# Optimization experiments

Hardware: AMD Instinct MI355X
Metric: run time of the kernel (lower is better)

The kernel has to match this reference:

```python
import jax, jax.numpy as jnp
import numpy as np

L, H, NH, HD, F, B, S = 32, 1024, 16, 64, 2048, 2, 2048
HPH = H // NH  # hidden per attention head (hyena column split)
EPS = 1e-6
BLOCK = {0:'HCS',4:'HCS',7:'HCS',11:'HCS',14:'HCS',18:'HCS',21:'HCS',25:'HCS',28:'HCS',
         1:'HCM',5:'HCM',8:'HCM',12:'HCM',15:'HCM',19:'HCM',22:'HCM',26:'HCM',29:'HCM',
         2:'HCL',6:'HCL',9:'HCL',13:'HCL',16:'HCL',20:'HCL',23:'HCL',27:'HCL',30:'HCL',
         3:'ATT',10:'ATT',17:'ATT',24:'ATT',31:'ATT'}

def rmsnorm(x, w):
    return x * jax.lax.rsqrt(jnp.mean(x * x, -1, keepdims=True) + EPS) * w

def step_fir(u, state, w, b, flip=False, gated=False):
    # u:[B,C]  state:[B,C,cache]  w:[C,Lf]  b:[C]  (single-token FIR step)
    cache = state.shape[-1]
    w = w[:, ::-1][:, -(cache + 1):] if flip else w[:, :cache + 1]
    y = w[:, -1] * u + jnp.sum(state * w[:, :-1], -1)
    y = y + (b * u if gated else b)
    return y

def split3(z):
    # column_split_hyena=True path of _interleave_split
    r = z.reshape(z.shape[0], NH, 3 * HPH)
    x2 = r[:, :, :HPH].reshape(z.shape[0], H)
    x1 = r[:, :, HPH:2 * HPH].reshape(z.shape[0], H)
    v = r[:, :, 2 * HPH:].reshape(z.shape[0], H)
    return x2, x1, v

def mlp(x, W1, W2):
    return jax.nn.gelu(x @ W1.T) @ W2.T

def fir_block(x, n1, n2, pW, pb, oW, ob, W1, W2, sfw, sfb, h, D, fstate, istate, flip, gated):
    xn = rmsnorm(x, n1)
    z = xn @ pW.T + pb                 # [B,1,3H]
    u = z[:, -1]                       # [B,3H]
    zp = step_fir(u, fstate, sfw, sfb)
    x2, x1, v = split3(zp)
    y = step_fir(x1 * v, istate, h, D, flip=flip, gated=gated)
    y = (y * x2)[:, None]              # [B,1,H]
    x = y @ oW.T + ob + x
    return mlp(rmsnorm(x, n2), W1, W2) + x

def hcl_block(x, n1, n2, pW, pb, oW, ob, W1, W2, sfw, sfb, log_poles, residues, D, fstate, iir):
    xn = rmsnorm(x, n1)
    z = xn @ pW.T + pb
    u = z[:, -1]
    zp = step_fir(u, fstate, sfw, sfb)
    x2, x1, v = split3(zp)
    x1v = x1 * v
    iir_new = jnp.exp(log_poles) * iir + x1v[..., None]   # [B,H,SS] single-step IIR update
    res = jnp.sum(residues * iir_new, -1)
    y = (x2 * (res + D * x1v))[:, None]
    x = y @ oW.T + ob + x
    return mlp(rmsnorm(x, n2), W1, W2) + x

def att_block(x, n1, n2, qW, qb, oW, ob, W1, W2, kc, vc, cos, sin, pos):
    xn = rmsnorm(x, n1)
    qkv = (xn @ qW.T + qb).reshape(B, 1, 3, NH, HD)
    q, k, v = qkv[:, :, 0], qkv[:, :, 1], qkv[:, :, 2]
    c = jnp.concatenate([cos[pos], cos[pos]])  # [HD]
    s = jnp.concatenate([sin[pos], sin[pos]])
    rot = lambda t: jnp.concatenate([-t[..., HD // 2:], t[..., :HD // 2]], -1)
    q = q * c + rot(q) * s
    k = k * c + rot(k) * s
    kc = kc.at[:, pos].set(k[:, 0])  # KV-cache scatter write at current position
    vc = vc.at[:, pos].set(v[:, 0])
    scores = jnp.einsum('bohd,bshd->bhos', q, kc) * (HD ** -0.5)
    scores = jnp.where(jnp.arange(S) > pos, -10000.0, scores)
    aw = jax.nn.softmax(scores, -1)
    ctx = jnp.einsum('bhos,bshd->bohd', aw, vc).reshape(B, 1, H)
    x = ctx @ oW.T + ob + x
    return mlp(rmsnorm(x, n2), W1, W2) + x

def forward(x, position, norm1_w, norm2_w, proj_W, proj_b, out_W, out_b, mlp_W1, mlp_W2,
            sf_w, sf_b, hcs_h, hcs_D, hcm_h, hcm_D, hcl_logpoles, hcl_residues, hcl_D,
            fir_state, hcs_state, hcm_state, iir_state, k_cache, v_cache, rope_cos, rope_sin):
    att = 0
    for i in range(L):  # loop over 32 structurally distinct layers (static)
        t = BLOCK[i]
        cm = (norm1_w[i], norm2_w[i], proj_W[i], proj_b[i], out_W[i], out_b[i], mlp_W1[i], mlp_W2[i])
        if t == 'HCS':
            x = fir_block(x, *cm, sf_w[i], sf_b[i], hcs_h[i], hcs_D[i], fir_state[i], hcs_state[i], False, False)
        elif t == 'HCM':
            x = fir_block(x, *cm, sf_w[i], sf_b[i], hcm_h[i], hcm_D[i], fir_state[i], hcm_state[i], True, True)
        elif t == 'HCL':
            x = hcl_block(x, *cm, sf_w[i], sf_b[i], hcl_logpoles[i], hcl_residues[i], hcl_D[i], fir_state[i], iir_state[i])
        else:
            x = att_block(x, *cm, k_cache[att], v_cache[att], rope_cos, rope_sin, position)
            att += 1
    return x

def setup_inputs():
    key = jax.random.key(0)
    ks = jax.random.split(key, 24)
    g = lambda k, shape, sc: jax.random.normal(k, shape, jnp.float32) * sc
    inv_freq = 1.0 / (10000.0 ** (np.arange(0, HD, 2, dtype=np.float32) / HD))
    ang = np.arange(S, dtype=np.float32)[:, None] * inv_freq[None, :]
    return {
        'x': g(ks[0], (B, 1, H), 1.0),
        'position': 1024,
        'norm1_w': jnp.ones((L, H), jnp.float32),
        'norm2_w': jnp.ones((L, H), jnp.float32),
        'proj_W': g(ks[1], (L, 3 * H, H), H ** -0.5),
        'proj_b': jnp.zeros((L, 3 * H), jnp.float32),
        'out_W': g(ks[2], (L, H, H), 0.2 * H ** -0.5),
        'out_b': jnp.zeros((L, H), jnp.float32),
        'mlp_W1': g(ks[3], (L, F, H), H ** -0.5),
        'mlp_W2': g(ks[4], (L, H, F), 0.2 * F ** -0.5),
        'sf_w': g(ks[5], (L, 3 * H, 3), 0.4),
        'sf_b': g(ks[6], (L, 3 * H), 0.02),
        'hcs_h': g(ks[7], (L, H, 7), 0.2),
        'hcs_D': g(ks[8], (L, H), 0.2),
        'hcm_h': g(ks[9], (L, H, 128), 0.04),
        'hcm_D': g(ks[10], (L, H), 0.2),
        'hcl_logpoles': -jax.random.uniform(ks[11], (L, H, 16), jnp.float32, 0.01, 2.0),
        'hcl_residues': g(ks[12], (L, H, 16), 0.1),
        'hcl_D': g(ks[13], (L, H), 0.2),
        'fir_state': g(ks[14], (L, B, 3 * H, 2), 0.5),
        'hcs_state': g(ks[15], (L, B, H, 6), 0.5),
        'hcm_state': g(ks[16], (L, B, H, 127), 0.5),
        'iir_state': g(ks[17], (L, B, H, 16), 0.5),
        'k_cache': g(ks[18], (5, B, S, NH, HD), 1.0),
        'v_cache': g(ks[19], (5, B, S, NH, HD), 1.0),
        'rope_cos': jnp.asarray(np.cos(ang)),
        'rope_sin': jnp.asarray(np.sin(ang)),
    }

def reference(x, position, norm1_w, norm2_w, proj_W, proj_b, out_W, out_b, mlp_W1, mlp_W2,
              sf_w, sf_b, hcs_h, hcs_D, hcm_h, hcm_D, hcl_logpoles, hcl_residues, hcl_D,
              fir_state, hcs_state, hcm_state, iir_state, k_cache, v_cache, rope_cos, rope_sin):
    return forward(x, position, norm1_w, norm2_w, proj_W, proj_b, out_W, out_b, mlp_W1, mlp_W2,
                   sf_w, sf_b, hcs_h, hcs_D, hcm_h, hcm_D, hcl_logpoles, hcl_residues, hcl_D,
                   fir_state, hcs_state, hcm_state, iir_state, k_cache, v_cache, rope_cos, rope_sin)
```

## Files before the change

### kernel.cpp

```cpp
#include <hip/hip_runtime.h>
#include <hip/hip_bf16.h>
#include <math.h>

#define LAYERS 32
#define H      1024
#define H3     3072
#define NHEADS 16
#define HDIM   64
#define FF     2048
#define BATCH  2
#define SEQ    2048
#define EPSF   1e-6f

__device__ __forceinline__ float wredSum(float v) {
#pragma unroll
  for (int m = 32; m >= 1; m >>= 1) v += __shfl_xor(v, m, 64);
  return v;
}
__device__ __forceinline__ float wredMax(float v) {
#pragma unroll
  for (int m = 32; m >= 1; m >>= 1) v = fmaxf(v, __shfl_xor(v, m, 64));
  return v;
}
__device__ __forceinline__ float gelu_t(float x) {
  return 0.5f * x * (1.0f + tanhf(0.7978845608028654f * (x + 0.044715f * x * x * x)));
}

__global__ __launch_bounds__(256) void prep_kernel(
    const float* __restrict__ sf_w, const float* __restrict__ sf_b,
    const float* __restrict__ fir_state,
    const float* __restrict__ hcs_h, const float* __restrict__ hcs_D, const float* __restrict__ hcs_state,
    const float* __restrict__ hcm_h, const float* __restrict__ hcm_D, const float* __restrict__ hcm_state,
    const float* __restrict__ lp, const float* __restrict__ resd, const float* __restrict__ hcl_D,
    const float* __restrict__ iir,
    unsigned long long kbits,
    float* __restrict__ sfd, float* __restrict__ sfc,
    float* __restrict__ mix0, float* __restrict__ mix1)
{
  int blk = blockIdx.x, tid = threadIdx.x;
  if (blk < 768) {
    int idx = blk * 256 + tid;
    int i = idx / (BATCH * H3);
    int r = idx % (BATCH * H3);
    int b = r / H3, ch = r % H3;
    const float* fs = fir_state + ((size_t)(i * BATCH + b) * H3 + ch) * 2;
    const float* sw = sf_w + ((size_t)i * H3 + ch) * 3;
    sfd[idx] = fs[0] * sw[0] + fs[1] * sw[1] + sf_b[i * H3 + ch];
    if (b == 0) sfc[i * H3 + ch] = sw[2];
  } else if (blk < 1024) {
    int idx = (blk - 768) * 256 + tid;
    int i = idx >> 11;
    int r = idx & 2047;
    int b = r >> 10, c = r & 1023;
    int kind = (int)((kbits >> (2 * i)) & 3ull);
    if (kind == 0) {
      const float* st = hcs_state + ((size_t)(i * BATCH + b) * H + c) * 6;
      const float* hh = hcs_h + ((size_t)i * H + c) * 7;
      float acc = 0.f;
#pragma unroll
      for (int k = 0; k < 6; k++) acc += st[k] * hh[k];
      mix0[idx] = acc + hcs_D[i * H + c];
      if (b == 0) mix1[i * H + c] = hh[6];
    } else if (kind == 2) {
      const float* ii = iir + ((size_t)(i * BATCH + b) * H + c) * 16;
      const float* lpp = lp + ((size_t)i * H + c) * 16;
      const float* rs = resd + ((size_t)i * H + c) * 16;
      float acc = 0.f, rsum = 0.f;
#pragma unroll
      for (int k = 0; k < 16; k++) { float rv = rs[k]; acc += rv * expf(lpp[k]) * ii[k]; rsum += rv; }
      mix0[idx] = acc;
      if (b == 0) mix1[i * H + c] = rsum + hcl_D[i * H + c];
    }
  } else {
    int w = tid >> 6, lane = tid & 63;
    int widx = (blk - 1024) * 4 + w;
    if (widx < 9 * BATCH * H) {
      int li = widx >> 11;
      int r = widx & 2047;
      int b = r >> 10, c = r & 1023;
      int i = (li >> 1) * 7 + ((li & 1) ? 5 : 1);
      const float* st = hcm_state + ((size_t)(i * BATCH + b) * H + c) * 127;
      const float* hh = hcm_h + ((size_t)i * H + c) * 128;
      float acc = 0.f;
      int k = lane;
      if (k < 127) acc += st[k] * hh[127 - k];
      k = lane + 64;
      if (k < 127) acc += st[k] * hh[127 - k];
      acc = wredSum(acc);
      if (lane == 0) {
        mix0[(i * BATCH + b) * H + c] = acc;
        if (b == 0) mix1[i * H + c] = hh[0] + hcm_D[i * H + c];
      }
    }
  }
}

template<int ROWS, bool GELU, bool HASBIAS>
__global__ __launch_bounds__(256) void gemv_norm_kernel(
    const float* __restrict__ x, const float* __restrict__ nw,
    const float* __restrict__ W, const float* __restrict__ bias,
    float* __restrict__ out)
{
  __shared__ alignas(16) float xe[BATCH][H];
  __shared__ float red[8];
  __shared__ float scl[BATCH];
  int tid = threadIdx.x, lane = tid & 63, w = tid >> 6;
  int r0 = blockIdx.x * 8 + w * 2;
  const float4* row0 = (const float4*)(W + (size_t)r0 * H);
  const float4* row1 = (const float4*)(W + (size_t)(r0 + 1) * H);
  float4 wa[4], wb[4];
#pragma unroll
  for (int j = 0; j < 4; j++) { wa[j] = row0[lane + 64 * j]; wb[j] = row1[lane + 64 * j]; }

  float ss0 = 0.f, ss1 = 0.f;
#pragma unroll
  for (int it = 0; it < 8; it++) {
    int e = tid + it * 256;
    int b = e >> 10, c = e & 1023;
    float xv = x[b * H + c];
    xe[b][c] = xv * nw[c];
    if (it < 4) ss0 += xv * xv; else ss1 += xv * xv;
  }
  ss0 = wredSum(ss0); ss1 = wredSum(ss1);
  if (lane == 0) { red[w] = ss0; red[4 + w] = ss1; }
  __syncthreads();
  if (tid == 0) {
    scl[0] = rsqrtf((red[0] + red[1] + red[2] + red[3]) * (1.0f / H) + EPSF);
    scl[1] = rsqrtf((red[4] + red[5] + red[6] + red[7]) * (1.0f / H) + EPSF);
  }
  __syncthreads();

  float a00 = 0.f, a01 = 0.f, a10 = 0.f, a11 = 0.f;
  const float4* x0 = (const float4*)xe[0];
  const float4* x1 = (const float4*)xe[1];
#pragma unroll
  for (int j = 0; j < 4; j++) {
    float4 h0 = x0[lane + 64 * j], h1 = x1[lane + 64 * j];
    a00 += wa[j].x * h0.x + wa[j].y * h0.y + wa[j].z * h0.z + wa[j].w * h0.w;
    a01 += wa[j].x * h1.x + wa[j].y * h1.y + wa[j].z * h1.z + wa[j].w * h1.w;
    a10 += wb[j].x * h0.x + wb[j].y * h0.y + wb[j].z * h0.z + wb[j].w * h0.w;
    a11 += wb[j].x * h1.x + wb[j].y * h1.y + wb[j].z * h1.z + wb[j].w * h1.w;
  }
  a00 = wredSum(a00); a01 = wredSum(a01); a10 = wredSum(a10); a11 = wredSum(a11);
  if (lane == 0) {
    float s0 = scl[0], s1 = scl[1];
    float b0 = HASBIAS ? bias[r0] : 0.f;
    float b1 = HASBIAS ? bias[r0 + 1] : 0.f;
    float v00 = a00 * s0 + b0, v01 = a01 * s1 + b0;
    float v10 = a10 * s0 + b1, v11 = a11 * s1 + b1;
    if (GELU) { v00 = gelu_t(v00); v01 = gelu_t(v01); v10 = gelu_t(v10); v11 = gelu_t(v11); }
    out[0 * ROWS + r0] = v00;
    out[1 * ROWS + r0] = v01;
    out[0 * ROWS + r0 + 1] = v10;
    out[1 * ROWS + r0 + 1] = v11;
  }
}

__global__ __launch_bounds__(256) void mix_out_kernel(
    int kind,
    const float* __restrict__ z, const float* __restrict__ sfdL, const float* __restrict__ sfcL,
    const float* __restrict__ mix0L, const float* __restrict__ mix1L,
    const float* __restrict__ attP,
    const float* __restrict__ oW, const float* __restrict__ ob,
    const float* __restrict__ x_in, float* __restrict__ x_out)
{
  __shared__ alignas(16) float y[BATCH][H];
  int tid = threadIdx.x, lane = tid & 63, w = tid >> 6;
  int r0 = blockIdx.x * 8 + w * 2;
  const float4* row0 = (const float4*)(oW + (size_t)r0 * H);
  const float4* row1 = (const float4*)(oW + (size_t)(r0 + 1) * H);
  float4 wa[4], wb[4];
#pragma unroll
  for (int j = 0; j < 4; j++) { wa[j] = row0[lane + 64 * j]; wb[j] = row1[lane + 64 * j]; }

  if (kind < 3) {
#pragma unroll
    for (int it = 0; it < 8; it++) {
      int e = tid + it * 256;
      int b = e >> 10, c = e & 1023;
      int n = c >> 6, d = c & 63;
      int base = n * 192 + d;
      float x2 = sfcL[base] * z[b * H3 + base] + sfdL[b * H3 + base];
      float x1 = sfcL[base + 64] * z[b * H3 + base + 64] + sfdL[b * H3 + base + 64];
      float vv = sfcL[base + 128] * z[b * H3 + base + 128] + sfdL[b * H3 + base + 128];
      float t = x1 * vv;
      y[b][c] = (mix1L[c] * t + mix0L[b * H + c]) * x2;
    }
  } else {
#pragma unroll
    for (int it = 0; it < 8; it++) {
      int e = tid + it * 256;
      int b = e >> 10, c = e & 1023;
      int n = c >> 6, d = c & 63;
      float M = -1e30f;
#pragma unroll
      for (int sp = 0; sp < 8; sp++) M = fmaxf(M, attP[((sp * BATCH + b) * NHEADS + n) * 66 + 64]);
      float Ls = 0.f, num = 0.f;
#pragma unroll
      for (int sp = 0; sp < 8; sp++) {
        const float* P = attP + ((sp * BATCH + b) * NHEADS + n) * 66;
        float wgt = expf(P[64] - M);
        Ls += wgt * P[65];
        num += wgt * P[d];
      }
      y[b][c] = num / Ls;
    }
  }
  __syncthreads();

  float a00 = 0.f, a01 = 0.f, a10 = 0.f, a11 = 0.f;
  const float4* y0 = (const float4*)y[0];
  const float4* y1 = (const float4*)y[1];
#pragma unroll
  for (int j = 0; j < 4; j++) {
    float4 h0 = y0[lane + 64 * j], h1 = y1[lane + 64 * j];
    a00 += wa[j].x * h0.x + wa[j].y * h0.y + wa[j].z * h0.z + wa[j].w * h0.w;
    a01 += wa[j].x * h1.x + wa[j].y * h1.y + wa[j].z * h1.z + wa[j].w * h1.w;
    a10 += wb[j].x * h0.x + wb[j].y * h0.y + wb[j].z * h0.z + wb[j].w * h0.w;
    a11 += wb[j].x * h1.x + wb[j].y * h1.y + wb[j].z * h1.z + wb[j].w * h1.w;
  }
  a00 = wredSum(a00); a01 = wredSum(a01); a10 = wredSum(a10); a11 = wredSum(a11);
  if (lane == 0) {
    x_out[0 * H + r0]     = a00 + ob[r0]     + x_in[0 * H + r0];
    x_out[1 * H + r0]     = a01 + ob[r0]     + x_in[1 * H + r0];
    x_out[0 * H + r0 + 1] = a10 + ob[r0 + 1] + x_in[0 * H + r0 + 1];
    x_out[1 * H + r0 + 1] = a11 + ob[r0 + 1] + x_in[1 * H + r0 + 1];
  }
}

__global__ __launch_bounds__(256) void gemv_mlp2_kernel(
    const float* __restrict__ h, const float* __restrict__ W2,
    const float* __restrict__ x_in, float* __restrict__ x_out)
{
  __shared__ alignas(16) float hs[BATCH][FF];
  int tid = threadIdx.x, lane = tid & 63, w = tid >> 6;
  int r = blockIdx.x * 4 + w;
  const float4* row = (const float4*)(W2 + (size_t)r * FF);
  float4 wv[8];
#pragma unroll
  for (int j = 0; j < 8; j++) wv[j] = row[lane + 64 * j];
#pragma unroll
  for (int it = 0; it < 16; it++) {
    int e = tid + it * 256;
    int b = e >> 11, c = e & 2047;
    hs[b][c] = h[b * FF + c];
  }
  __syncthreads();
  float a0 = 0.f, a1 = 0.f;
  const float4* h0 = (const float4*)hs[0];
  const float4* h1 = (const float4*)hs[1];
#pragma unroll
  for (int j = 0; j < 8; j++) {
    float4 p = h0[lane + 64 * j], q = h1[lane + 64 * j];
    a0 += wv[j].x * p.x + wv[j].y * p.y + wv[j].z * p.z + wv[j].w * p.w;
    a1 += wv[j].x * q.x + wv[j].y * q.y + wv[j].z * q.z + wv[j].w * q.w;
  }
  a0 = wredSum(a0); a1 = wredSum(a1);
  if (lane == 0) {
    x_out[0 * H + r] = a0 + x_in[0 * H + r];
    x_out[1 * H + r] = a1 + x_in[1 * H + r];
  }
}

__global__ __launch_bounds__(256) void attn_kernel(
    const float* __restrict__ z, const int* __restrict__ posp,
    const float* __restrict__ kc, const float* __restrict__ vc,
    const float* __restrict__ cosT, const float* __restrict__ sinT,
    float* __restrict__ P)
{
  int sp = blockIdx.x & 7, n = (blockIdx.x >> 3) & 15, b = blockIdx.x >> 7;
  int pos = *posp;
  __shared__ alignas(16) float q_s[HDIM], k_s[HDIM], v_s[HDIM];
  __shared__ float eg[256];
  __shared__ float redA[4];
  __shared__ alignas(16) float osum[4][HDIM];
  int tid = threadIdx.x, lane = tid & 63, w = tid >> 6;

  if (tid < 64) {
    int d = tid, j = d & 31;
    float cs = cosT[pos * 32 + j], sn = sinT[pos * 32 + j];
    float qv = z[b * H3 + n * 64 + d];
    float qo = z[b * H3 + n * 64 + ((d + 32) & 63)];
    q_s[d] = ((d < 32) ? (qv * cs - qo * sn) : (qv * cs + qo * sn)) * 0.125f;
    float kv = z[b * H3 + 1024 + n * 64 + d];
    float ko = z[b * H3 + 1024 + n * 64 + ((d + 32) & 63)];
    k_s[d] = (d < 32) ? (kv * cs - ko * sn) : (kv * cs + ko * sn);
    v_s[d] = z[b * H3 + 2048 + n * 64 + d];
  }
  __syncthreads();

  int s = sp * 256 + tid;
  float logit = -1e30f;
  if (s <= pos) {
    const float4* k4 = (s == pos) ? (const float4*)k_s
                                  : (const float4*)(kc + (((size_t)b * SEQ + s) * NHEADS + n) * HDIM);
    const float4* q4 = (const float4*)q_s;
    float acc = 0.f;
#pragma unroll
    for (int j = 0; j < 16; j++) {
      float4 kk = k4[j], qq = q4[j];
      acc += kk.x * qq.x + kk.y * qq.y + kk.z * qq.z + kk.w * qq.w;
    }
    logit = acc;
  }
  float m = wredMax(logit);
  if (lane == 0) redA[w] = m;
  __syncthreads();
  m = fmaxf(fmaxf(redA[0], redA[1]), fmaxf(redA[2], redA[3]));
  float e = (s <= pos) ? expf(logit - m) : 0.f;
  eg[tid] = e;
  float ps = wredSum(e);
  __syncthreads();
  if (lane == 0) redA[w] = ps;
  __syncthreads();
  float lsum = redA[0] + redA[1] + redA[2] + redA[3];

  int dgrp = lane & 15, srow = lane >> 4;
  float4 acc = make_float4(0.f, 0.f, 0.f, 0.f);
#pragma unroll 4
  for (int it = 0; it < 16; it++) {
    int sl = w * 64 + it * 4;
    if (sp * 256 + sl > pos) break;
    int sli = sl + srow;
    int ss = sp * 256 + sli;
    float ev = eg[sli];
    const float4* v4 = (ss == pos) ? (const float4*)v_s
                                   : (const float4*)(vc + (((size_t)b * SEQ + ss) * NHEADS + n) * HDIM);
    float4 vv = v4[dgrp];
    acc.x += ev * vv.x; acc.y += ev * vv.y; acc.z += ev * vv.z; acc.w += ev * vv.w;
  }
#pragma unroll
  for (int mm = 16; mm <= 32; mm <<= 1) {
    acc.x += __shfl_xor(acc.x, mm, 64);
    acc.y += __shfl_xor(acc.y, mm, 64);
    acc.z += __shfl_xor(acc.z, mm, 64);
    acc.w += __shfl_xor(acc.w, mm, 64);
  }
  if (srow == 0) ((float4*)osum[w])[dgrp] = acc;
  __syncthreads();
  float* Pp = P + ((size_t)(sp * BATCH + b) * NHEADS + n) * 66;
  if (tid < 64) Pp[tid] = osum[0][tid] + osum[1][tid] + osum[2][tid] + osum[3][tid];
  if (tid == 64) Pp[64] = m;
  if (tid == 65) Pp[65] = lsum;
}

extern "C" void kernel_launch(void* const* d_in, const int* in_sizes, int n_in,
                              void* d_out, int out_size, void* d_ws, size_t ws_size,
                              hipStream_t stream) {
  (void)in_sizes; (void)n_in; (void)out_size; (void)ws_size;
  const float* x0    = (const float*)d_in[0];
  const int*   posp  = (const int*)d_in[1];
  const float* n1    = (const float*)d_in[2];
  const float* n2    = (const float*)d_in[3];
  const float* pW    = (const float*)d_in[4];
  const float* pb    = (const float*)d_in[5];
  const float* oW    = (const float*)d_in[6];
  const float* ob    = (const float*)d_in[7];
  const float* W1    = (const float*)d_in[8];
  const float* W2    = (const float*)d_in[9];
  const float* sfw   = (const float*)d_in[10];
  const float* sfb   = (const float*)d_in[11];
  const float* hcs_h = (const float*)d_in[12];
  const float* hcs_D = (const float*)d_in[13];
  const float* hcm_h = (const float*)d_in[14];
  const float* hcm_D = (const float*)d_in[15];
  const float* lp    = (const float*)d_in[16];
  const float* resd  = (const float*)d_in[17];
  const float* hclD  = (const float*)d_in[18];
  const float* fir   = (const float*)d_in[19];
  const float* hcsS  = (const float*)d_in[20];
  const float* hcmS  = (const float*)d_in[21];
  const float* iir   = (const float*)d_in[22];
  const float* kc    = (const float*)d_in[23];
  const float* vc    = (const float*)d_in[24];
  const float* cosT  = (const float*)d_in[25];
  const float* sinT  = (const float*)d_in[26];

  float* ws    = (float*)d_ws;
  float* xbuf0 = ws;
  float* xbuf1 = ws + 2048;
  float* zbuf  = ws + 4096;
  float* hbuf  = ws + 10240;
  float* attP  = ws + 14336;
  float* sfd   = ws + 31232;
  float* sfc   = ws + 227840;
  float* mix0  = ws + 326144;
  float* mix1  = ws + 391680;

  static const int KIND[LAYERS] = {0,1,2,3,0,1,2,0,1,2,3,0,1,2,0,1,2,3,0,1,2,0,1,2,3,0,1,2,0,1,2,3};
  unsigned long long kbits = 0ull;
  for (int i = 0; i < LAYERS; i++) kbits |= ((unsigned long long)KIND[i]) << (2 * i);

  prep_kernel<<<5632, 256, 0, stream>>>(sfw, sfb, fir, hcs_h, hcs_D, hcsS,
      hcm_h, hcm_D, hcmS, lp, resd, hclD, iir, kbits, sfd, sfc, mix0, mix1);

  const float* xsrc = x0;
  int att = 0;
  for (int i = 0; i < LAYERS; i++) {
    gemv_norm_kernel<H3, false, true><<<H3 / 8, 256, 0, stream>>>(
        xsrc, n1 + i * H, pW + (size_t)i * H3 * H, pb + i * H3, zbuf);
    if (KIND[i] == 3) {
      attn_kernel<<<256, 256, 0, stream>>>(
          zbuf, posp, kc + (size_t)att * BATCH * SEQ * NHEADS * HDIM,
          vc + (size_t)att * BATCH * SEQ * NHEADS * HDIM, cosT, sinT, attP);
      att++;
    }
    mix_out_kernel<<<H / 8, 256, 0, stream>>>(
        KIND[i], zbuf, sfd + (size_t)i * BATCH * H3, sfc + (size_t)i * H3,
        mix0 + (size_t)i * BATCH * H, mix1 + (size_t)i * H, attP,
        oW + (size_t)i * H * H, ob + i * H, xsrc, xbuf1);
    gemv_norm_kernel<FF, true, false><<<FF / 8, 256, 0, stream>>>(
        xbuf1, n2 + i * H, W1 + (size_t)i * FF * H, nullptr, hbuf);
    gemv_mlp2_kernel<<<H / 4, 256, 0, stream>>>(
        hbuf, W2 + (size_t)i * H * FF, xbuf1, (i == 31) ? (float*)d_out : xbuf0);
    xsrc = xbuf0;
  }
}
```

Before: 702.8 us.

## Replace per-layer kernel launches with a persistent cooperative megakernel using grid barriers

Replaces the roughly 130 small per-layer kernel launches with one persistent cooperative kernel that walks all 32 layers. Stages are separated by a custom atomic grid barrier whose counters prep_kernel zeroes. The hyena FIR/mix elementwise step is fused into the projection GEMV epilogue, with projection rows reordered so each block gets matching x2/x1/v rows. Attention is re-split into 512 tasks. This removes launch overhead and inter-kernel gaps, but adds barrier spin costs and relies on all workgroups being co-resident.

```diff
diff --git a/kernel.cpp b/kernel.cpp
--- a/kernel.cpp
+++ b/kernel.cpp
@@ -11,6 +11,9 @@
 #define BATCH  2
 #define SEQ    2048
 #define EPSF   1e-6f
+#define NBAR   160
+
+__constant__ int d_KIND[LAYERS] = {0,1,2,3,0,1,2,0,1,2,3,0,1,2,0,1,2,3,0,1,2,0,1,2,3,0,1,2,0,1,2,3};
 
 __device__ __forceinline__ float wredSum(float v) {
 #pragma unroll
@@ -24,6 +27,369 @@
 }
 __device__ __forceinline__ float gelu_t(float x) {
   return 0.5f * x * (1.0f + tanhf(0.7978845608028654f * (x + 0.044715f * x * x * x)));
+}
+
+struct NS   { float xe[2][1024]; float red[16]; float scl[2]; float p[6][4][2]; };
+struct W2S  { float hs[2][2048]; float pr[2][8][2]; };
+struct OUTS { float ys[2][1024]; float pr[2][4][2]; };
+struct ATTS { float q[64]; float k[64]; float v[64]; float e[128]; float red[16]; float osum[8][64]; };
+union SH { NS ns; W2S w2; OUTS o; ATTS att; };
+
+struct MegaArgs {
+  const float* x0; const int* posp;
+  const float* n1; const float* n2;
+  const float* pW; const float* pb; const float* oW; const float* ob;
+  const float* W1; const float* W2;
+  const float* sfc; const float* sfd; const float* mix0; const float* mix1;
+  const float* kc; const float* vc; const float* cosT; const float* sinT;
+  float* z; float* y; float* xA; float* xB; float* xM; float* h; float* attP;
+  int* bar; float* out; int nwg;
+};
+
+__device__ __forceinline__ void gridbar(int* bar, int st, int wg, int nwg) {
+  __syncthreads();
+  if (threadIdx.x == 0) {
+    int* cnt  = bar + st * 8;
+    int* flag = bar + NBAR * 8 + st;
+    __hip_atomic_fetch_add(&cnt[wg & 7], 1, __ATOMIC_RELEASE, __HIP_MEMORY_SCOPE_AGENT);
+    if (wg == 0) {
+      int s;
+      do {
+        s = 0;
+#pragma unroll
+        for (int i = 0; i < 8; i++)
+          s += __hip_atomic_load(&cnt[i], __ATOMIC_RELAXED, __HIP_MEMORY_SCOPE_AGENT);
+      } while (s < nwg);
+      __hip_atomic_store(flag, 1, __ATOMIC_RELEASE, __HIP_MEMORY_SCOPE_AGENT);
+    } else {
+      while (__hip_atomic_load(flag, __ATOMIC_RELAXED, __HIP_MEMORY_SCOPE_AGENT) == 0) {}
+    }
+    __builtin_amdgcn_fence(__ATOMIC_ACQUIRE, "agent");
+  }
+  __syncthreads();
+}
+
+__device__ __forceinline__ void block_norm(const float* __restrict__ xin,
+                                           const float* __restrict__ nw, SH& sh) {
+  int tid = threadIdx.x, lane = tid & 63, wave = tid >> 6;
+  float4 xv = ((const float4*)xin)[tid];
+  int b = tid >> 8, ci = tid & 255;
+  float4 nv = ((const float4*)nw)[ci];
+  float ss = xv.x * xv.x + xv.y * xv.y + xv.z * xv.z + xv.w * xv.w;
+  ((float4*)&sh.ns.xe[b][ci << 2])[0] =
+      make_float4(xv.x * nv.x, xv.y * nv.y, xv.z * nv.z, xv.w * nv.w);
+  ss = wredSum(ss);
+  if (lane == 0) sh.ns.red[wave] = ss;
+  __syncthreads();
+  if (threadIdx.x == 0) {
+    sh.ns.scl[0] = rsqrtf((sh.ns.red[0] + sh.ns.red[1] + sh.ns.red[2] + sh.ns.red[3]) * (1.0f / 1024.f) + EPSF);
+    sh.ns.scl[1] = rsqrtf((sh.ns.red[4] + sh.ns.red[5] + sh.ns.red[6] + sh.ns.red[7]) * (1.0f / 1024.f) + EPSF);
+  }
+  __syncthreads();
+}
+
+__device__ __forceinline__ void stageP(const MegaArgs& a, SH& sh, int wg, int nwg,
+                                       int layer, int kind, const float* xin) {
+  block_norm(xin, a.n1 + layer * H, sh);
+  const float* W  = a.pW + (size_t)layer * H3 * H;
+  const float* pb = a.pb + layer * H3;
+  const float* sfcL = a.sfc + (size_t)layer * H3;
+  const float* sfdL = a.sfd + (size_t)layer * 2 * H3;
+  const float* mix0L = a.mix0 + (size_t)layer * 2 * H;
+  const float* mix1L = a.mix1 + (size_t)layer * H;
+  int tid = threadIdx.x, lane = tid & 63, wave = tid >> 6;
+  for (int rb = wg; rb < 512; rb += nwg) {
+    int n = rb >> 5, d0 = (rb & 31) << 1;
+    float part[3][2];
+    float4 wv[3];
+#pragma unroll
+    for (int k = 0; k < 3; k++) {
+      int t = wave + 8 * k, j = t >> 2, ch = t & 3;
+      int grow = (kind == 3) ? (rb * 6 + j) : (n * 192 + (j >> 1) * 64 + d0 + (j & 1));
+      wv[k] = *(const float4*)(W + (size_t)grow * H + (ch << 8) + (lane << 2));
+    }
+#pragma unroll
+    for (int k = 0; k < 3; k++) {
+      int ch = (wave + 8 * k) & 3;
+      float4 xa = *(const float4*)&sh.ns.xe[0][(ch << 8) + (lane << 2)];
+      float4 xb = *(const float4*)&sh.ns.xe[1][(ch << 8) + (lane << 2)];
+      part[k][0] = wv[k].x * xa.x + wv[k].y * xa.y + wv[k].z * xa.z + wv[k].w * xa.w;
+      part[k][1] = wv[k].x * xb.x + wv[k].y * xb.y + wv[k].z * xb.z + wv[k].w * xb.w;
+    }
+#pragma unroll
+    for (int k = 0; k < 3; k++) {
+      float s0 = wredSum(part[k][0]);
+      float s1 = wredSum(part[k][1]);
+      int t = wave + 8 * k, j = t >> 2, ch = t & 3;
+      if (lane == 0) { sh.ns.p[j][ch][0] = s0; sh.ns.p[j][ch][1] = s1; }
+    }
+    __syncthreads();
+    if (wave == 0) {
+      if (lane < 48) {
+        int j = lane >> 3, b = (lane >> 2) & 1, ch = lane & 3;
+        float v = sh.ns.p[j][ch][b];
+        v += __shfl_xor(v, 1, 64);
+        v += __shfl_xor(v, 2, 64);
+        if (ch == 0) {
+          int grow = (kind == 3) ? (rb * 6 + j) : (n * 192 + (j >> 1) * 64 + d0 + (j & 1));
+          float zraw = v * sh.ns.scl[b] + pb[grow];
+          if (kind == 3) {
+            a.z[b * H3 + grow] = zraw;
+          } else {
+            sh.ns.p[j][0][b] = sfcL[grow] * zraw + sfdL[b * H3 + grow];
+          }
+        }
+      }
+      if (kind != 3 && lane < 4) {
+        int q = lane & 1, b = lane >> 1;
+        float x2 = sh.ns.p[0 + q][0][b];
+        float x1 = sh.ns.p[2 + q][0][b];
+        float vv = sh.ns.p[4 + q][0][b];
+        int c = n * 64 + d0 + q;
+        float t = x1 * vv;
+        a.y[b * H + c] = (mix1L[c] * t + mix0L[b * H + c]) * x2;
+      }
+    }
+    __syncthreads();
+  }
+}
+
+__device__ __forceinline__ void stageA(const MegaArgs& a, SH& sh, int wg, int nwg, int att) {
+  int tid = threadIdx.x, lane = tid & 63;
+  int pos = a.posp[0];
+  int ck = (pos + 16) >> 4;
+  const float* kcL = a.kc + (size_t)att * BATCH * SEQ * NHEADS * HDIM;
+  const float* vcL = a.vc + (size_t)att * BATCH * SEQ * NHEADS * HDIM;
+  for (int task = wg; task < 512; task += nwg) {
+    int sp = task & 15, n = (task >> 4) & 15, b = task >> 8;
+    int s0 = sp * ck;
+    int send = min(s0 + ck, pos + 1);
+    if (tid < 64) {
+      int d = tid, jr = d & 31;
+      float cs = a.cosT[pos * 32 + jr], sn = a.sinT[pos * 32 + jr];
+      float qv = a.z[b * H3 + n * 64 + d];
+      float qo = a.z[b * H3 + n * 64 + ((d + 32) & 63)];
+      sh.att.q[d] = ((d < 32) ? (qv * cs - qo * sn) : (qv * cs + qo * sn)) * 0.125f;
+      float kv = a.z[b * H3 + 1024 + n * 64 + d];
+      float ko = a.z[b * H3 + 1024 + n * 64 + ((d + 32) & 63)];
+      sh.att.k[d] = (d < 32) ? (kv * cs - ko * sn) : (kv * cs + ko * sn);
+      sh.att.v[d] = a.z[b * H3 + 2048 + n * 64 + d];
+    }
+    __syncthreads();
+    int slot = tid >> 2, quarter = tid & 3;
+    int p = s0 + slot;
+    float lg = -1e30f;
+    if (p < send) {
+      const float4* k4 = (p == pos) ? (const float4*)sh.att.k
+                                    : (const float4*)(kcL + (((size_t)b * SEQ + p) * NHEADS + n) * HDIM);
+      const float4* q4 = (const float4*)sh.att.q;
+      float acc = 0.f;
+#pragma unroll
+      for (int jj = 0; jj < 4; jj++) {
+        float4 kk = k4[quarter * 4 + jj], qq = q4[quarter * 4 + jj];
+        acc += kk.x * qq.x + kk.y * qq.y + kk.z * qq.z + kk.w * qq.w;
+      }
+      acc += __shfl_xor(acc, 1, 64);
+      acc += __shfl_xor(acc, 2, 64);
+      lg = acc;
+    }
+    float mw = wredMax(lg);
+    if (lane == 0) sh.att.red[tid >> 6] = mw;
+    __syncthreads();
+    float m = sh.att.red[0];
+#pragma unroll
+    for (int jj = 1; jj < 8; jj++) m = fmaxf(m, sh.att.red[jj]);
+    float ee = expf(lg - m);
+    if (quarter == 0) sh.att.e[slot] = ee;
+    float ssum = wredSum(quarter == 0 ? ee : 0.f);
+    __syncthreads();
+    if (lane == 0) sh.att.red[tid >> 6] = ssum;
+    __syncthreads();
+    float lsum = 0.f;
+#pragma unroll
+    for (int jj = 0; jj < 8; jj++) lsum += sh.att.red[jj];
+    int d = tid & 63, prow = tid >> 6;
+    float acc2 = 0.f;
+    for (int jj = prow; jj < ck; jj += 8) {
+      int pp = s0 + jj;
+      if (pp < send) {
+        const float* vrow = (pp == pos) ? sh.att.v
+                                        : (vcL + (((size_t)b * SEQ + pp) * NHEADS + n) * HDIM);
+        acc2 += sh.att.e[jj] * vrow[d];
+      }
+    }
+    sh.att.osum[prow][d] = acc2;
+    __syncthreads();
+    float* Pp = a.attP + (size_t)task * 66;
+    if (tid < 64) {
+      float o = 0.f;
+#pragma unroll
+      for (int jj = 0; jj < 8; jj++) o += sh.att.osum[jj][d];
+      Pp[d] = o;
+    } else if (tid == 64) Pp[64] = m;
+    else if (tid == 65) Pp[65] = lsum;
+    __syncthreads();
+  }
+}
+
+__device__ __forceinline__ void stageOut(const MegaArgs& a, SH& sh, int wg, int nwg,
+                                         int layer, int kind, const float* xin) {
+  int tid = threadIdx.x, lane = tid & 63, wave = tid >> 6;
+  if (kind != 3) {
+    for (int e = tid; e < 2048; e += 512) (&sh.o.ys[0][0])[e] = a.y[e];
+  } else {
+    for (int e = tid; e < 2048; e += 512) {
+      int b = e >> 10, c = e & 1023, n = c >> 6, d = c & 63;
+      const float* P = a.attP + (size_t)((b * 16 + n) * 16) * 66;
+      float M = -1e30f;
+#pragma unroll
+      for (int sp = 0; sp < 16; sp++) M = fmaxf(M, P[sp * 66 + 64]);
+      float L = 0.f, num = 0.f;
+#pragma unroll
+      for (int sp = 0; sp < 16; sp++) {
+        float w = expf(P[sp * 66 + 64] - M);
+        L += w * P[sp * 66 + 65];
+        num += w * P[sp * 66 + d];
+      }
+      (&sh.o.ys[0][0])[e] = num / L;
+    }
+  }
+  __syncthreads();
+  const float* W  = a.oW + (size_t)layer * H * H;
+  const float* ob = a.ob + layer * H;
+  for (int rb = wg; rb < 512; rb += nwg) {
+    int j = wave >> 2, ch = wave & 3;
+    int grow = rb * 2 + j;
+    float4 wv = *(const float4*)(W + (size_t)grow * H + (ch << 8) + (lane << 2));
+    float4 ya = *(const float4*)&sh.o.ys[0][(ch << 8) + (lane << 2)];
+    float4 yb = *(const float4*)&sh.o.ys[1][(ch << 8) + (lane << 2)];
+    float p0 = wv.x * ya.x + wv.y * ya.y + wv.z * ya.z + wv.w * ya.w;
+    float p1 = wv.x * yb.x + wv.y * yb.y + wv.z * yb.z + wv.w * yb.w;
+    p0 = wredSum(p0); p1 = wredSum(p1);
+    if (lane == 0) { sh.o.pr[j][ch][0] = p0; sh.o.pr[j][ch][1] = p1; }
+    __syncthreads();
+    if (wave == 0 && lane < 16) {
+      int jj = lane >> 3, b = (lane >> 2) & 1, cc = lane & 3;
+      float v = sh.o.pr[jj][cc][b];
+      v += __shfl_xor(v, 1, 64);
+      v += __shfl_xor(v, 2, 64);
+      if (cc == 0) {
+        int gr = rb * 2 + jj;
+        a.xM[b * H + gr] = v + ob[gr] + xin[b * H + gr];
+      }
+    }
+    __syncthreads();
+  }
+}
+
+__device__ __forceinline__ void stageW1(const MegaArgs& a, SH& sh, int wg, int nwg, int layer) {
+  block_norm(a.xM, a.n2 + layer * H, sh);
+  const float* W = a.W1 + (size_t)layer * FF * H;
+  int tid = threadIdx.x, lane = tid & 63, wave = tid >> 6;
+  for (int rb = wg; rb < 512; rb += nwg) {
+    float part[2][2];
+    float4 wv[2];
+#pragma unroll
+    for (int k = 0; k < 2; k++) {
+      int t = wave + 8 * k, j = t >> 2, ch = t & 3;
+      wv[k] = *(const float4*)(W + (size_t)(rb * 4 + j) * H + (ch << 8) + (lane << 2));
+    }
+#pragma unroll
+    for (int k = 0; k < 2; k++) {
+      int ch = (wave + 8 * k) & 3;
+      float4 xa = *(const float4*)&sh.ns.xe[0][(ch << 8) + (lane << 2)];
+      float4 xb = *(const float4*)&sh.ns.xe[1][(ch << 8) + (lane << 2)];
+      part[k][0] = wv[k].x * xa.x + wv[k].y * xa.y + wv[k].z * xa.z + wv[k].w * xa.w;
+      part[k][1] = wv[k].x * xb.x + wv[k].y * xb.y + wv[k].z * xb.z + wv[k].w * xb.w;
+    }
+#pragma unroll
+    for (int k = 0; k < 2; k++) {
+      float s0 = wredSum(part[k][0]);
+      float s1 = wredSum(part[k][1]);
+      int t = wave + 8 * k, j = t >> 2, ch = t & 3;
+      if (lane == 0) { sh.ns.p[j][ch][0] = s0; sh.ns.p[j][ch][1] = s1; }
+    }
+    __syncthreads();
+    if (wave == 0 && lane < 32) {
+      int j = lane >> 3, b = (lane >> 2) & 1, ch = lane & 3;
+      float v = sh.ns.p[j][ch][b];
+      v += __shfl_xor(v, 1, 64);
+      v += __shfl_xor(v, 2, 64);
+      if (ch == 0) a.h[b * FF + rb * 4 + j] = gelu_t(v * sh.ns.scl[b]);
+    }
+    __syncthreads();
+  }
+}
+
+__device__ __forceinline__ void stageW2(const MegaArgs& a, SH& sh, int wg, int nwg,
+                                        int layer, float* xout) {
+  int tid = threadIdx.x, lane = tid & 63, wave = tid >> 6;
+  for (int e = tid; e < 4096; e += 512) (&sh.w2.hs[0][0])[e] = a.h[e];
+  __syncthreads();
+  const float* W = a.W2 + (size_t)layer * H * FF;
+  for (int rb = wg; rb < 512; rb += nwg) {
+    float part[2][2];
+    float4 wv[2];
+#pragma unroll
+    for (int k = 0; k < 2; k++) {
+      int t = wave + 8 * k, j = t >> 3, ch = t & 7;
+      wv[k] = *(const float4*)(W + (size_t)(rb * 2 + j) * FF + (ch << 8) + (lane << 2));
+    }
+#pragma unroll
+    for (int k = 0; k < 2; k++) {
+      int ch = (wave + 8 * k) & 7;
+      float4 ha = *(const float4*)&sh.w2.hs[0][(ch << 8) + (lane << 2)];
+      float4 hb = *(const float4*)&sh.w2.hs[1][(ch << 8) + (lane << 2)];
+      part[k][0] = wv[k].x * ha.x + wv[k].y * ha.y + wv[k].z * ha.z + wv[k].w * ha.w;
+      part[k][1] = wv[k].x * hb.x + wv[k].y * hb.y + wv[k].z * hb.z + wv[k].w * hb.w;
+    }
+#pragma unroll
+    for (int k = 0; k < 2; k++) {
+      float s0 = wredSum(part[k][0]);
+      float s1 = wredSum(part[k][1]);
+      int t = wave + 8 * k, j = t >> 3, ch = t & 7;
+      if (lane == 0) { sh.w2.pr[j][ch][0] = s0; sh.w2.pr[j][ch][1] = s1; }
+    }
+    __syncthreads();
+    if (wave == 0 && lane < 32) {
+      int j = lane >> 4, b = (lane >> 3) & 1, ch = lane & 7;
+      float v = sh.w2.pr[j][ch][b];
+      v += __shfl_xor(v, 1, 64);
+      v += __shfl_xor(v, 2, 64);
+      v += __shfl_xor(v, 4, 64);
+      if (ch == 0) {
+        int gr = rb * 2 + j;
+        xout[b * H + gr] = v + a.xM[b * H + gr];
+      }
+    }
+    __syncthreads();
+  }
+}
+
+__global__ __launch_bounds__(512, 4) void mega(MegaArgs a) {
+  __shared__ SH sh;
+  int wg = blockIdx.x, nwg = a.nwg;
+  int st = 0;
+  const float* xin = a.x0;
+  int att = 0;
+  for (int i = 0; i < LAYERS; i++) {
+    int kind = d_KIND[i];
+    stageP(a, sh, wg, nwg, i, kind, xin);
+    gridbar(a.bar, st++, wg, nwg);
+    if (kind == 3) {
+      stageA(a, sh, wg, nwg, att);
+      gridbar(a.bar, st++, wg, nwg);
+      att++;
+    }
+    stageOut(a, sh, wg, nwg, i, kind, xin);
+    gridbar(a.bar, st++, wg, nwg);
+    stageW1(a, sh, wg, nwg, i);
+    gridbar(a.bar, st++, wg, nwg);
+    float* xout = (i == LAYERS - 1) ? a.out : ((i & 1) ? a.xB : a.xA);
+    stageW2(a, sh, wg, nwg, i, xout);
+    if (i != LAYERS - 1) gridbar(a.bar, st++, wg, nwg);
+    xin = xout;
+  }
 }
 
 __global__ __launch_bounds__(256) void prep_kernel(
@@ -35,7 +401,7 @@
     const float* __restrict__ iir,
     unsigned long long kbits,
     float* __restrict__ sfd, float* __restrict__ sfc,
-    float* __restrict__ mix0, float* __restrict__ mix1)
+    float* __restrict__ mix0, float* __restrict__ mix1, int* __restrict__ bar)
 {
   int blk = blockIdx.x, tid = threadIdx.x;
   if (blk < 768) {
@@ -71,7 +437,7 @@
       mix0[idx] = acc;
       if (b == 0) mix1[i * H + c] = rsum + hcl_D[i * H + c];
     }
-  } else {
+  } else if (blk < 5632) {
     int w = tid >> 6, lane = tid & 63;
     int widx = (blk - 1024) * 4 + w;
     if (widx < 9 * BATCH * H) {
@@ -92,256 +458,9 @@
         if (b == 0) mix1[i * H + c] = hh[0] + hcm_D[i * H + c];
       }
     }
-  }
-}
-
-template<int ROWS, bool GELU, bool HASBIAS>
-__global__ __launch_bounds__(256) void gemv_norm_kernel(
-    const float* __restrict__ x, const float* __restrict__ nw,
-    const float* __restrict__ W, const float* __restrict__ bias,
-    float* __restrict__ out)
-{
-  __shared__ alignas(16) float xe[BATCH][H];
-  __shared__ float red[8];
-  __shared__ float scl[BATCH];
-  int tid = threadIdx.x, lane = tid & 63, w = tid >> 6;
-  int r0 = blockIdx.x * 8 + w * 2;
-  const float4* row0 = (const float4*)(W + (size_t)r0 * H);
-  const float4* row1 = (const float4*)(W + (size_t)(r0 + 1) * H);
-  float4 wa[4], wb[4];
-#pragma unroll
-  for (int j = 0; j < 4; j++) { wa[j] = row0[lane + 64 * j]; wb[j] = row1[lane + 64 * j]; }
-
-  float ss0 = 0.f, ss1 = 0.f;
-#pragma unroll
-  for (int it = 0; it < 8; it++) {
-    int e = tid + it * 256;
-    int b = e >> 10, c = e & 1023;
-    float xv = x[b * H + c];
-    xe[b][c] = xv * nw[c];
-    if (it < 4) ss0 += xv * xv; else ss1 += xv * xv;
-  }
-  ss0 = wredSum(ss0); ss1 = wredSum(ss1);
-  if (lane == 0) { red[w] = ss0; red[4 + w] = ss1; }
-  __syncthreads();
-  if (tid == 0) {
-    scl[0] = rsqrtf((red[0] + red[1] + red[2] + red[3]) * (1.0f / H) + EPSF);
-    scl[1] = rsqrtf((red[4] + red[5] + red[6] + red[7]) * (1.0f / H) + EPSF);
-  }
-  __syncthreads();
-
-  float a00 = 0.f, a01 = 0.f, a10 = 0.f, a11 = 0.f;
-  const float4* x0 = (const float4*)xe[0];
-  const float4* x1 = (const float4*)xe[1];
-#pragma unroll
-  for (int j = 0; j < 4; j++) {
-    float4 h0 = x0[lane + 64 * j], h1 = x1[lane + 64 * j];
-    a00 += wa[j].x * h0.x + wa[j].y * h0.y + wa[j].z * h0.z + wa[j].w * h0.w;
-    a01 += wa[j].x * h1.x + wa[j].y * h1.y + wa[j].z * h1.z + wa[j].w * h1.w;
-    a10 += wb[j].x * h0.x + wb[j].y * h0.y + wb[j].z * h0.z + wb[j].w * h0.w;
-    a11 += wb[j].x * h1.x + wb[j].y * h1.y + wb[j].z * h1.z + wb[j].w * h1.w;
-  }
-  a00 = wredSum(a00); a01 = wredSum(a01); a10 = wredSum(a10); a11 = wredSum(a11);
-  if (lane == 0) {
-    float s0 = scl[0], s1 = scl[1];
-    float b0 = HASBIAS ? bias[r0] : 0.f;
-    float b1 = HASBIAS ? bias[r0 + 1] : 0.f;
-    float v00 = a00 * s0 + b0, v01 = a01 * s1 + b0;
-    float v10 = a10 * s0 + b1, v11 = a11 * s1 + b1;
-    if (GELU) { v00 = gelu_t(v00); v01 = gelu_t(v01); v10 = gelu_t(v10); v11 = gelu_t(v11); }
-    out[0 * ROWS + r0] = v00;
-    out[1 * ROWS + r0] = v01;
-    out[0 * ROWS + r0 + 1] = v10;
-    out[1 * ROWS + r0 + 1] = v11;
-  }
-}
-
-__global__ __launch_bounds__(256) void mix_out_kernel(
-    int kind,
-    const float* __restrict__ z, const float* __restrict__ sfdL, const float* __restrict__ sfcL,
-    const float* __restrict__ mix0L, const float* __restrict__ mix1L,
-    const float* __restrict__ attP,
-    const float* __restrict__ oW, const float* __restrict__ ob,
-    const float* __restrict__ x_in, float* __restrict__ x_out)
-{
-  __shared__ alignas(16) float y[BATCH][H];
-  int tid = threadIdx.x, lane = tid & 63, w = tid >> 6;
-  int r0 = blockIdx.x * 8 + w * 2;
-  const float4* row0 = (const float4*)(oW + (size_t)r0 * H);
-  const float4* row1 = (const float4*)(oW + (size_t)(r0 + 1) * H);
-  float4 wa[4], wb[4];
-#pragma unroll
-  for (int j = 0; j < 4; j++) { wa[j] = row0[lane + 64 * j]; wb[j] = row1[lane + 64 * j]; }
-
-  if (kind < 3) {
-#pragma unroll
-    for (int it = 0; it < 8; it++) {
-      int e = tid + it * 256;
-      int b = e >> 10, c = e & 1023;
-      int n = c >> 6, d = c & 63;
-      int base = n * 192 + d;
-      float x2 = sfcL[base] * z[b * H3 + base] + sfdL[b * H3 + base];
-      float x1 = sfcL[base + 64] * z[b * H3 + base + 64] + sfdL[b * H3 + base + 64];
-      float vv = sfcL[base + 128] * z[b * H3 + base + 128] + sfdL[b * H3 + base + 128];
-      float t = x1 * vv;
-      y[b][c] = (mix1L[c] * t + mix0L[b * H + c]) * x2;
-    }
   } else {
-#pragma unroll
-    for (int it = 0; it < 8; it++) {
-      int e = tid + it * 256;
-      int b = e >> 10, c = e & 1023;
-      int n = c >> 6, d = c & 63;
-      float M = -1e30f;
-#pragma unroll
-      for (int sp = 0; sp < 8; sp++) M = fmaxf(M, attP[((sp * BATCH + b) * NHEADS + n) * 66 + 64]);
-      float Ls = 0.f, num = 0.f;
-#pragma unroll
-      for (int sp = 0; sp < 8; sp++) {
-        const float* P = attP + ((sp * BATCH + b) * NHEADS + n) * 66;
-        float wgt = expf(P[64] - M);
-        Ls += wgt * P[65];
-        num += wgt * P[d];
-      }
-      y[b][c] = num / Ls;
-    }
-  }
-  __syncthreads();
-
-  float a00 = 0.f, a01 = 0.f, a10 = 0.f, a11 = 0.f;
-  const float4* y0 = (const float4*)y[0];
-  const float4* y1 = (const float4*)y[1];
-#pragma unroll
-  for (int j = 0; j < 4; j++) {
-    float4 h0 = y0[lane + 64 * j], h1 = y1[lane + 64 * j];
-    a00 += wa[j].x * h0.x + wa[j].y * h0.y + wa[j].z * h0.z + wa[j].w * h0.w;
-    a01 += wa[j].x * h1.x + wa[j].y * h1.y + wa[j].z * h1.z + wa[j].w * h1.w;
-    a10 += wb[j].x * h0.x + wb[j].y * h0.y + wb[j].z * h0.z + wb[j].w * h0.w;
-    a11 += wb[j].x * h1.x + wb[j].y * h1.y + wb[j].z * h1.z + wb[j].w * h1.w;
-  }
-  a00 = wredSum(a00); a01 = wredSum(a01); a10 = wredSum(a10); a11 = wredSum(a11);
-  if (lane == 0) {
-    x_out[0 * H + r0]     = a00 + ob[r0]     + x_in[0 * H + r0];
-    x_out[1 * H + r0]     = a01 + ob[r0]     + x_in[1 * H + r0];
-    x_out[0 * H + r0 + 1] = a10 + ob[r0 + 1] + x_in[0 * H + r0 + 1];
-    x_out[1 * H + r0 + 1] = a11 + ob[r0 + 1] + x_in[1 * H + r0 + 1];
-  }
-}
-
-__global__ __launch_bounds__(256) void gemv_mlp2_kernel(
-    const float* __restrict__ h, const float* __restrict__ W2,
-    const float* __restrict__ x_in, float* __restrict__ x_out)
-{
-  __shared__ alignas(16) float hs[BATCH][FF];
-  int tid = threadIdx.x, lane = tid & 63, w = tid >> 6;
-  int r = blockIdx.x * 4 + w;
-  const float4* row = (const float4*)(W2 + (size_t)r * FF);
-  float4 wv[8];
-#pragma unroll
-  for (int j = 0; j < 8; j++) wv[j] = row[lane + 64 * j];
-#pragma unroll
-  for (int it = 0; it < 16; it++) {
-    int e = tid + it * 256;
-    int b = e >> 11, c = e & 2047;
-    hs[b][c] = h[b * FF + c];
-  }
-  __syncthreads();
-  float a0 = 0.f, a1 = 0.f;
-  const float4* h0 = (const float4*)hs[0];
-  const float4* h1 = (const float4*)hs[1];
-#pragma unroll
-  for (int j = 0; j < 8; j++) {
-    float4 p = h0[lane + 64 * j], q = h1[lane + 64 * j];
-    a0 += wv[j].x * p.x + wv[j].y * p.y + wv[j].z * p.z + wv[j].w * p.w;
-    a1 += wv[j].x * q.x + wv[j].y * q.y + wv[j].z * q.z + wv[j].w * q.w;
-  }
-  a0 = wredSum(a0); a1 = wredSum(a1);
-  if (lane == 0) {
-    x_out[0 * H + r] = a0 + x_in[0 * H + r];
-    x_out[1 * H + r] = a1 + x_in[1 * H + r];
-  }
-}
-
-__global__ __launch_bounds__(256) void attn_kernel(
-    const float* __restrict__ z, const int* __restrict__ posp,
-    const float* __restrict__ kc, const float* __restrict__ vc,
-    const float* __restrict__ cosT, const float* __restrict__ sinT,
-    float* __restrict__ P)
-{
-  int sp = blockIdx.x & 7, n = (blockIdx.x >> 3) & 15, b = blockIdx.x >> 7;
-  int pos = *posp;
-  __shared__ alignas(16) float q_s[HDIM], k_s[HDIM], v_s[HDIM];
-  __shared__ float eg[256];
-  __shared__ float redA[4];
-  __shared__ alignas(16) float osum[4][HDIM];
-  int tid = threadIdx.x, lane = tid & 63, w = tid >> 6;
-
-  if (tid < 64) {
-    int d = tid, j = d & 31;
-    float cs = cosT[pos * 32 + j], sn = sinT[pos * 32 + j];
-    float qv = z[b * H3 + n * 64 + d];
-    float qo = z[b * H3 + n * 64 + ((d + 32) & 63)];
-    q_s[d] = ((d < 32) ? (qv * cs - qo * sn) : (qv * cs + qo * sn)) * 0.125f;
-    float kv = z[b * H3 + 1024 + n * 64 + d];
-    float ko = z[b * H3 + 1024 + n * 64 + ((d + 32) & 63)];
-    k_s[d] = (d < 32) ? (kv * cs - ko * sn) : (kv * cs + ko * sn);
-    v_s[d] = z[b * H3 + 2048 + n * 64 + d];
-  }
-  __syncthreads();
-
-  int s = sp * 256 + tid;
-  float logit = -1e30f;
-  if (s <= pos) {
-    const float4* k4 = (s == pos) ? (const float4*)k_s
-                                  : (const float4*)(kc + (((size_t)b * SEQ + s) * NHEADS + n) * HDIM);
-    const float4* q4 = (const float4*)q_s;
-    float acc = 0.f;
-#pragma unroll
-    for (int j = 0; j < 16; j++) {
-      float4 kk = k4[j], qq = q4[j];
-      acc += kk.x * qq.x + kk.y * qq.y + kk.z * qq.z + kk.w * qq.w;
-    }
-    logit = acc;
-  }
-  float m = wredMax(logit);
-  if (lane == 0) redA[w] = m;
-  __syncthreads();
-  m = fmaxf(fmaxf(redA[0], redA[1]), fmaxf(redA[2], redA[3]));
-  float e = (s <= pos) ? expf(logit - m) : 0.f;
-  eg[tid] = e;
-  float ps = wredSum(e);
-  __syncthreads();
-  if (lane == 0) redA[w] = ps;
-  __syncthreads();
-  float lsum = redA[0] + redA[1] + redA[2] + redA[3];
-
-  int dgrp = lane & 15, srow = lane >> 4;
-  float4 acc = make_float4(0.f, 0.f, 0.f, 0.f);
-#pragma unroll 4
-  for (int it = 0; it < 16; it++) {
-    int sl = w * 64 + it * 4;
-    if (sp * 256 + sl > pos) break;
-    int sli = sl + srow;
-    int ss = sp * 256 + sli;
-    float ev = eg[sli];
-    const float4* v4 = (ss == pos) ? (const float4*)v_s
-                                   : (const float4*)(vc + (((size_t)b * SEQ + ss) * NHEADS + n) * HDIM);
-    float4 vv = v4[dgrp];
-    acc.x += ev * vv.x; acc.y += ev * vv.y; acc.z += ev * vv.z; acc.w += ev * vv.w;
-  }
-#pragma unroll
-  for (int mm = 16; mm <= 32; mm <<= 1) {
-    acc.x += __shfl_xor(acc.x, mm, 64);
-    acc.y += __shfl_xor(acc.y, mm, 64);
-    acc.z += __shfl_xor(acc.z, mm, 64);
-    acc.w += __shfl_xor(acc.w, mm, 64);
-  }
-  if (srow == 0) ((float4*)osum[w])[dgrp] = acc;
-  __syncthreads();
-  float* Pp = P + ((size_t)(sp * BATCH + b) * NHEADS + n) * 66;
-  if (tid < 64) Pp[tid] = osum[0][tid] + osum[1][tid] + osum[2][tid] + osum[3][tid];
-  if (tid == 64) Pp[64] = m;
-  if (tid == 65) Pp[65] = lsum;
+    for (int j = tid; j < NBAR * 9; j += 256) bar[j] = 0;
+  }
 }
 
 extern "C" void kernel_launch(void* const* d_in, const int* in_sizes, int n_in,
@@ -376,43 +495,41 @@
   const float* cosT  = (const float*)d_in[25];
   const float* sinT  = (const float*)d_in[26];
 
-  float* ws    = (float*)d_ws;
-  float* xbuf0 = ws;
-  float* xbuf1 = ws + 2048;
-  float* zbuf  = ws + 4096;
-  float* hbuf  = ws + 10240;
-  float* attP  = ws + 14336;
-  float* sfd   = ws + 31232;
-  float* sfc   = ws + 227840;
-  float* mix0  = ws + 326144;
-  float* mix1  = ws + 391680;
+  float* ws   = (float*)d_ws;
+  float* xA   = ws;
+  float* xB   = ws + 2048;
+  float* xM   = ws + 4096;
+  float* zb   = ws + 6144;
+  float* yb   = ws + 12288;
+  float* hb   = ws + 14336;
+  float* attP = ws + 18432;
+  float* sfd  = ws + 52224;
+  float* sfc  = ws + 248832;
+  float* mix0 = ws + 347136;
+  float* mix1 = ws + 412672;
+  int*   bar  = (int*)(ws + 445440);
 
   static const int KIND[LAYERS] = {0,1,2,3,0,1,2,0,1,2,3,0,1,2,0,1,2,3,0,1,2,0,1,2,3,0,1,2,0,1,2,3};
   unsigned long long kbits = 0ull;
   for (int i = 0; i < LAYERS; i++) kbits |= ((unsigned long long)KIND[i]) << (2 * i);
 
-  prep_kernel<<<5632, 256, 0, stream>>>(sfw, sfb, fir, hcs_h, hcs_D, hcsS,
-      hcm_h, hcm_D, hcmS, lp, resd, hclD, iir, kbits, sfd, sfc, mix0, mix1);
-
-  const float* xsrc = x0;
-  int att = 0;
-  for (int i = 0; i < LAYERS; i++) {
-    gemv_norm_kernel<H3, false, true><<<H3 / 8, 256, 0, stream>>>(
-        xsrc, n1 + i * H, pW + (size_t)i * H3 * H, pb + i * H3, zbuf);
-    if (KIND[i] == 3) {
-      attn_kernel<<<256, 256, 0, stream>>>(
-          zbuf, posp, kc + (size_t)att * BATCH * SEQ * NHEADS * HDIM,
-          vc + (size_t)att * BATCH * SEQ * NHEADS * HDIM, cosT, sinT, attP);
-      att++;
-    }
-    mix_out_kernel<<<H / 8, 256, 0, stream>>>(
-        KIND[i], zbuf, sfd + (size_t)i * BATCH * H3, sfc + (size_t)i * H3,
-        mix0 + (size_t)i * BATCH * H, mix1 + (size_t)i * H, attP,
-        oW + (size_t)i * H * H, ob + i * H, xsrc, xbuf1);
-    gemv_norm_kernel<FF, true, false><<<FF / 8, 256, 0, stream>>>(
-        xbuf1, n2 + i * H, W1 + (size_t)i * FF * H, nullptr, hbuf);
-    gemv_mlp2_kernel<<<H / 4, 256, 0, stream>>>(
-        hbuf, W2 + (size_t)i * H * FF, xbuf1, (i == 31) ? (float*)d_out : xbuf0);
-    xsrc = xbuf0;
-  }
-}
+  prep_kernel<<<5633, 256, 0, stream>>>(sfw, sfb, fir, hcs_h, hcs_D, hcsS,
+      hcm_h, hcm_D, hcmS, lp, resd, hclD, iir, kbits, sfd, sfc, mix0, mix1, bar);
+
+  int occ = 0;
+  hipError_t oe = hipOccupancyMaxActiveBlocksPerMultiprocessor(&occ, mega, 512, 0);
+  if (oe != hipSuccess || occ < 1) occ = 1;
+  int nwg = occ * 256;
+  if (nwg > 512) nwg = 512;
+
+  MegaArgs ma;
+  ma.x0 = x0; ma.posp = posp; ma.n1 = n1; ma.n2 = n2;
+  ma.pW = pW; ma.pb = pb; ma.oW = oW; ma.ob = ob; ma.W1 = W1; ma.W2 = W2;
+  ma.sfc = sfc; ma.sfd = sfd; ma.mix0 = mix0; ma.mix1 = mix1;
+  ma.kc = kc; ma.vc = vc; ma.cosT = cosT; ma.sinT = sinT;
+  ma.z = zb; ma.y = yb; ma.xA = xA; ma.xB = xB; ma.xM = xM; ma.h = hb; ma.attP = attP;
+  ma.bar = bar; ma.out = (float*)d_out; ma.nwg = nwg;
+
+  void* kp[] = { &ma };
+  hipLaunchCooperativeKernel(mega, dim3(nwg), dim3(512), kp, 0, stream);
+}
```

New measurement: 1.828 ms. 160% more time.
